# Optimization experiments

Measured on AMD Instinct MI355X. Metric: run time of the kernel, lower is better.

The kernel has to match this reference:

```python
import jax, jax.numpy as jnp
import numpy as np

N_CAND = 10   # n_point_candidate
SIGMA = 1.0   # std threshold for vote filtering
EPS = 1e-6


def _get_pt_candidates(pcld, kpts_ofst, seg, cpt_ofst, k):
    # pcld [b,n,3]; kpts_ofst [b,n,8,3]; seg [b,n,1]; cpt_ofst [b,n,1,3]
    offsets = jnp.concatenate([kpts_ofst, cpt_ofst], axis=2)        # [b,n,9,3]
    scores = jnp.squeeze(seg, axis=-1)                              # [b,n]
    _, idx = jax.lax.top_k(scores, k)                               # [b,k] most confident points
    cands = pcld[:, :, None, :] + offsets                           # [b,n,9,3] candidate kpt positions
    cands = jnp.take_along_axis(cands, idx[:, :, None, None], axis=1)  # [b,k,9,3]
    return jnp.transpose(cands, (0, 2, 1, 3))                       # [b,9,k,3]


def _pts_clustering_with_std(kpts_cans, sigma=SIGMA):
    # kpts_cans [b,n_kpts,k,3]: keep candidates within sigma*std of the mean, average survivors
    mean = jnp.mean(kpts_cans, axis=2, keepdims=True)
    std = jnp.std(kpts_cans, axis=2, keepdims=True)
    inlier = jnp.all(jnp.abs(kpts_cans - mean) <= sigma * std, axis=-1)  # [b,n_kpts,k]
    w = inlier.astype(kpts_cans.dtype)[..., None]
    return jnp.sum(kpts_cans * w, axis=2) / (jnp.sum(w, axis=2) + EPS)   # [b,n_kpts,3]


def _rt_svd_transform(A, B, w):
    # Weighted Kabsch: find R,t with R @ A + t ~= B.  A,B [b,n,3]; w [n]
    wn = w / jnp.sum(w)
    cA = jnp.einsum('n,bnc->bc', wn, A)[:, None, :]                 # weighted centroids
    cB = jnp.einsum('n,bnc->bc', wn, B)[:, None, :]
    Am, Bm = A - cA, B - cB
    H = jnp.einsum('bni,n,bnj->bij', Am, w, Bm)                     # [b,3,3] cross-covariance
    U, S, Vh = jnp.linalg.svd(H)
    V = jnp.swapaxes(Vh, -1, -2)
    R0 = V @ jnp.swapaxes(U, -1, -2)
    flip = jnp.where(jnp.linalg.det(R0) < 0.0, -1.0, 1.0)           # reflection fix
    V = V.at[:, :, -1].multiply(flip[:, None])
    R = V @ jnp.swapaxes(U, -1, -2)                                 # [b,3,3]
    t = jnp.swapaxes(cB, -1, -2) - R @ jnp.swapaxes(cA, -1, -2)     # [b,3,1]
    return R, t


def setup_inputs() -> dict:
    key = jax.random.key(0)
    k1, k2, k3, k4, k5 = jax.random.split(key, 5)
    b, n, nk = 64, 12288, 8
    return {
        'pcld_input': jax.random.normal(k1, (b, n, 3), jnp.float32),
        'kpts_pre_input': jax.random.normal(k2, (b, n, nk, 3), jnp.float32),
        'cpt_pre_input': jax.random.normal(k3, (b, n, 1, 3), jnp.float32),
        'seg_pre_input': jax.random.uniform(k4, (b, n, 1), jnp.float32),
        'mesh_kpts_input': jax.random.normal(k5, (b, nk + 1, 3), jnp.float32),
    }


def reference(pcld_input, kpts_pre_input, cpt_pre_input, seg_pre_input, mesh_kpts_input):
    obj_kpts = _get_pt_candidates(pcld_input, kpts_pre_input, seg_pre_input, cpt_pre_input, N_CAND)
    kpts_voted = _pts_clustering_with_std(obj_kpts)                 # [b,9,3]
    n_pts = kpts_voted.shape[1]
    weights_vector = jnp.ones((n_pts,), dtype=kpts_voted.dtype)
    batch_R, batch_t = _rt_svd_transform(mesh_kpts_input, kpts_voted, weights_vector)
    batch_t = jnp.reshape(batch_t, (-1, 3))
    return batch_R, batch_t, kpts_voted
```

## Files before the change

kernel.cpp:

```cpp
#include <hip/hip_runtime.h>
#include <math.h>

#define NB      64
#define NPTS    12288
#define KTOP    10
#define NKP     9
#define T       1024
#define NWAVES  (T / 64)
#define PERTHD  (NPTS / T)

struct Pair { float v; int i; };

__device__ __forceinline__ bool better(const Pair& a, const Pair& b) {
    return (a.v > b.v) || (a.v == b.v && a.i < b.i);
}

__device__ __forceinline__ void ce(Pair& x, Pair& y) {
    if (better(y, x)) { Pair t = x; x = y; y = t; }
}

template <int LEN>
__device__ __forceinline__ void lane_sort_desc(Pair (&L)[LEN]) {
    #pragma unroll
    for (int r = 0; r < LEN; ++r) {
        #pragma unroll
        for (int i = 0; i + 1 < LEN; i += 2) {
            if ((r & 1) == 0) ce(L[i], L[i + 1]);
        }
        #pragma unroll
        for (int i = 1; i + 1 < LEN; i += 2) {
            if ((r & 1) == 1) ce(L[i], L[i + 1]);
        }
    }
}

template <int LEN>
__device__ __forceinline__ void wave_topk(Pair (&L)[LEN], Pair (&out)[KTOP]) {
    #pragma unroll
    for (int k = 0; k < KTOP; ++k) {
        Pair w = L[0];
        #pragma unroll
        for (int s = 1; s < 64; s <<= 1) {
            Pair o;
            o.v = __shfl_xor(w.v, s);
            o.i = __shfl_xor(w.i, s);
            if (better(o, w)) w = o;
        }
        out[k] = w;
        if (L[0].v == w.v && L[0].i == w.i) {
            #pragma unroll
            for (int i = 0; i + 1 < LEN; ++i) L[i] = L[i + 1];
            L[LEN - 1].v = -INFINITY; L[LEN - 1].i = 0x7fffffff;
        }
    }
}

__global__ __launch_bounds__(T)
void pose_fused(const float* __restrict__ pcld,
                const float* __restrict__ kpts,
                const float* __restrict__ cpt,
                const float* __restrict__ seg,
                const float* __restrict__ mesh,
                float* __restrict__ out)
{
    const int b = blockIdx.x;
    const int t = threadIdx.x;
    const int lane = t & 63;
    const int w = t >> 6;

    __shared__ Pair  wavetop[NWAVES][KTOP];
    __shared__ int   topidx[KTOP];
    __shared__ float cands[NKP][KTOP][3];
    __shared__ float voted[NKP][3];

    const float4* segb4 = (const float4*)(seg + (size_t)b * NPTS);
    Pair L[PERTHD];
    #pragma unroll
    for (int j = 0; j < 3; ++j) {
        int f4 = t + j * T;
        float4 a = segb4[f4];
        L[4 * j + 0] = {a.x, 4 * f4 + 0};
        L[4 * j + 1] = {a.y, 4 * f4 + 1};
        L[4 * j + 2] = {a.z, 4 * f4 + 2};
        L[4 * j + 3] = {a.w, 4 * f4 + 3};
    }
    lane_sort_desc<PERTHD>(L);

    Pair wt[KTOP];
    wave_topk<PERTHD>(L, wt);
    if (lane == 0) {
        #pragma unroll
        for (int j = 0; j < KTOP; ++j) wavetop[w][j] = wt[j];
    }
    __syncthreads();

    if (w == 0) {
        Pair M[KTOP];
        if (lane < NWAVES) {
            #pragma unroll
            for (int j = 0; j < KTOP; ++j) M[j] = wavetop[lane][j];
        } else {
            #pragma unroll
            for (int j = 0; j < KTOP; ++j) { M[j].v = -INFINITY; M[j].i = 0x7fffffff; }
        }
        Pair top[KTOP];
        wave_topk<KTOP>(M, top);
        if (lane == 0) {
            #pragma unroll
            for (int j = 0; j < KTOP; ++j) topidx[j] = top[j].i;
        }
    }
    __syncthreads();

    if (t < NKP * KTOP) {
        int j = t / KTOP;
        int i = t % KTOP;
        int p = topidx[i];
        size_t base = (size_t)b * NPTS + p;
        float px = pcld[base * 3 + 0], py = pcld[base * 3 + 1], pz = pcld[base * 3 + 2];
        float ox, oy, oz;
        if (j < 8) {
            size_t kb = (base * 8 + j) * 3;
            ox = kpts[kb + 0]; oy = kpts[kb + 1]; oz = kpts[kb + 2];
        } else {
            size_t cb = base * 3;
            ox = cpt[cb + 0]; oy = cpt[cb + 1]; oz = cpt[cb + 2];
        }
        cands[j][i][0] = px + ox;
        cands[j][i][1] = py + oy;
        cands[j][i][2] = pz + oz;
    }
    __syncthreads();

    if (t < NKP) {
        float mean[3] = {0.f, 0.f, 0.f};
        for (int i = 0; i < KTOP; ++i)
            for (int c = 0; c < 3; ++c) mean[c] += cands[t][i][c];
        for (int c = 0; c < 3; ++c) mean[c] *= (1.0f / KTOP);
        float var[3] = {0.f, 0.f, 0.f};
        for (int i = 0; i < KTOP; ++i)
            for (int c = 0; c < 3; ++c) { float d = cands[t][i][c] - mean[c]; var[c] += d * d; }
        float sd[3];
        for (int c = 0; c < 3; ++c) sd[c] = sqrtf(var[c] * (1.0f / KTOP));
        float wsum = 0.f, acc[3] = {0.f, 0.f, 0.f};
        for (int i = 0; i < KTOP; ++i) {
            bool in = true;
            for (int c = 0; c < 3; ++c) in = in && (fabsf(cands[t][i][c] - mean[c]) <= sd[c]);
            if (in) {
                wsum += 1.f;
                for (int c = 0; c < 3; ++c) acc[c] += cands[t][i][c];
            }
        }
        float inv = 1.f / (wsum + 1e-6f);
        for (int c = 0; c < 3; ++c) {
            float v = acc[c] * inv;
            voted[t][c] = v;
            out[NB * 9 + NB * 3 + ((size_t)b * NKP + t) * 3 + c] = v;
        }
    }
    __syncthreads();

    if (t == 0) {
        const float* mb = mesh + (size_t)b * NKP * 3;
        float A[NKP][3], Bv[NKP][3];
        float cA[3] = {0, 0, 0}, cB[3] = {0, 0, 0};
        for (int n = 0; n < NKP; ++n) {
            for (int c = 0; c < 3; ++c) {
                A[n][c]  = mb[n * 3 + c];
                Bv[n][c] = voted[n][c];
                cA[c] += A[n][c];
                cB[c] += Bv[n][c];
            }
        }
        for (int c = 0; c < 3; ++c) { cA[c] *= (1.0f / NKP); cB[c] *= (1.0f / NKP); }

        float H[3][3] = {{0,0,0},{0,0,0},{0,0,0}};
        for (int n = 0; n < NKP; ++n)
            for (int i = 0; i < 3; ++i)
                for (int j = 0; j < 3; ++j)
                    H[i][j] += (A[n][i] - cA[i]) * (Bv[n][j] - cB[j]);

        float Km[3][3];
        for (int i = 0; i < 3; ++i)
            for (int j = 0; j < 3; ++j) {
                float s = 0;
                for (int l = 0; l < 3; ++l) s += H[l][i] * H[l][j];
                Km[i][j] = s;
            }

        float V[3][3] = {{1,0,0},{0,1,0},{0,0,1}};
        for (int sweep = 0; sweep < 5; ++sweep) {
            for (int p = 0; p < 2; ++p) {
                for (int q = p + 1; q < 3; ++q) {
                    float apq = Km[p][q];
                    float app = Km[p][p], aqq = Km[q][q];
                    if (fabsf(apq) <= 1e-12f * (fabsf(app) + fabsf(aqq)) || apq == 0.0f) continue;
                    float theta = (aqq - app) / (2.0f * apq);
                    float tj = ((theta >= 0.0f) ? 1.0f : -1.0f) / (fabsf(theta) + sqrtf(theta * theta + 1.0f));
                    float cj = 1.0f / sqrtf(tj * tj + 1.0f);
                    float sj = tj * cj;
                    for (int l = 0; l < 3; ++l) {
                        float klp = Km[l][p], klq = Km[l][q];
                        Km[l][p] = cj * klp - sj * klq;
                        Km[l][q] = sj * klp + cj * klq;
                    }
                    for (int l = 0; l < 3; ++l) {
                        float kpl = Km[p][l], kql = Km[q][l];
                        Km[p][l] = cj * kpl - sj * kql;
                        Km[q][l] = sj * kpl + cj * kql;
                    }
                    for (int l = 0; l < 3; ++l) {
                        float vlp = V[l][p], vlq = V[l][q];
                        V[l][p] = cj * vlp - sj * vlq;
                        V[l][q] = sj * vlp + cj * vlq;
                    }
                }
            }
        }

        float eig[3] = {Km[0][0], Km[1][1], Km[2][2]};
        int ord[3] = {0, 1, 2};
        if (eig[ord[0]] < eig[ord[1]]) { int tmp = ord[0]; ord[0] = ord[1]; ord[1] = tmp; }
        if (eig[ord[1]] < eig[ord[2]]) { int tmp = ord[1]; ord[1] = ord[2]; ord[2] = tmp; }
        if (eig[ord[0]] < eig[ord[1]]) { int tmp = ord[0]; ord[0] = ord[1]; ord[1] = tmp; }

        float detH =
            H[0][0] * (H[1][1] * H[2][2] - H[1][2] * H[2][1]) -
            H[0][1] * (H[1][0] * H[2][2] - H[1][2] * H[2][0]) +
            H[0][2] * (H[1][0] * H[2][1] - H[1][1] * H[2][0]);
        float dsign[3] = {1.0f, 1.0f, (detH < 0.0f) ? -1.0f : 1.0f};

        float R[3][3] = {{0,0,0},{0,0,0},{0,0,0}};
        for (int k = 0; k < 3; ++k) {
            int c = ord[k];
            float s = sqrtf(fmaxf(eig[c], 0.0f));
            float invs = 1.0f / fmaxf(s, 1e-12f);
            float u[3];
            for (int l = 0; l < 3; ++l) {
                float a = 0;
                for (int m = 0; m < 3; ++m) a += H[l][m] * V[m][c];
                u[l] = a * invs;
            }
            for (int r = 0; r < 3; ++r)
                for (int cc = 0; cc < 3; ++cc)
                    R[r][cc] += dsign[k] * V[r][c] * u[cc];
        }

        float tv[3];
        for (int c = 0; c < 3; ++c) {
            float a = 0;
            for (int m = 0; m < 3; ++m) a += R[c][m] * cA[m];
            tv[c] = cB[c] - a;
        }

        for (int r = 0; r < 3; ++r)
            for (int c = 0; c < 3; ++c)
                out[(size_t)b * 9 + r * 3 + c] = R[r][c];
        for (int c = 0; c < 3; ++c)
            out[NB * 9 + (size_t)b * 3 + c] = tv[c];
    }
}

extern "C" void kernel_launch(void* const* d_in, const int* in_sizes, int n_in,
                              void* d_out, int out_size, void* d_ws, size_t ws_size,
                              hipStream_t stream) {
    const float* pcld = (const float*)d_in[0];
    const float* kpts = (const float*)d_in[1];
    const float* cpt  = (const float*)d_in[2];
    const float* seg  = (const float*)d_in[3];
    const float* mesh = (const float*)d_in[4];
    float* out = (float*)d_out;

    pose_fused<<<NB, T, 0, stream>>>(pcld, kpts, cpt, seg, mesh, out);
}
```

Measured before the change: 141.2 us.

## Replace per-lane sort top-k with threshold prefilter and packed 64-bit keys

The top-k selection over segmentation scores now keeps only values at or above a fixed threshold, collecting them into a small shared candidate list with atomics. One wave then picks the top 10 from that list using 64-bit packed value/index keys and max-shuffles. If the candidate count falls outside [KTOP, CAND_MAX], a wave-level exact scan of the whole row runs instead. This drops the per-lane odd-even sort and the two-level Pair reduction. It depends on the score distribution: non-negative floats compare correctly as packed keys, and the slow fallback path costs more when taken.

```diff
diff --git a/kernel.cpp b/kernel.cpp
--- a/kernel.cpp
+++ b/kernel.cpp
@@ -1,59 +1,21 @@
 #include <hip/hip_runtime.h>
 #include <math.h>
+
+typedef unsigned long long u64;
+typedef unsigned int u32;
 
 #define NB      64
 #define NPTS    12288
 #define KTOP    10
 #define NKP     9
 #define T       1024
-#define NWAVES  (T / 64)
-#define PERTHD  (NPTS / T)
-
-struct Pair { float v; int i; };
-
-__device__ __forceinline__ bool better(const Pair& a, const Pair& b) {
-    return (a.v > b.v) || (a.v == b.v && a.i < b.i);
+#define CAND_MAX 128
+#define THETA   0.997f
+
+__device__ __forceinline__ u64 pack(float v, int idx) {
+    return ((u64)__float_as_uint(v) << 32) | (u32)(~idx);
 }
-
-__device__ __forceinline__ void ce(Pair& x, Pair& y) {
-    if (better(y, x)) { Pair t = x; x = y; y = t; }
-}
-
-template <int LEN>
-__device__ __forceinline__ void lane_sort_desc(Pair (&L)[LEN]) {
-    #pragma unroll
-    for (int r = 0; r < LEN; ++r) {
-        #pragma unroll
-        for (int i = 0; i + 1 < LEN; i += 2) {
-            if ((r & 1) == 0) ce(L[i], L[i + 1]);
-        }
-        #pragma unroll
-        for (int i = 1; i + 1 < LEN; i += 2) {
-            if ((r & 1) == 1) ce(L[i], L[i + 1]);
-        }
-    }
-}
-
-template <int LEN>
-__device__ __forceinline__ void wave_topk(Pair (&L)[LEN], Pair (&out)[KTOP]) {
-    #pragma unroll
-    for (int k = 0; k < KTOP; ++k) {
-        Pair w = L[0];
-        #pragma unroll
-        for (int s = 1; s < 64; s <<= 1) {
-            Pair o;
-            o.v = __shfl_xor(w.v, s);
-            o.i = __shfl_xor(w.i, s);
-            if (better(o, w)) w = o;
-        }
-        out[k] = w;
-        if (L[0].v == w.v && L[0].i == w.i) {
-            #pragma unroll
-            for (int i = 0; i + 1 < LEN; ++i) L[i] = L[i + 1];
-            L[LEN - 1].v = -INFINITY; L[LEN - 1].i = 0x7fffffff;
-        }
-    }
-}
+__device__ __forceinline__ int unpack_idx(u64 p) { return (int)(~(u32)p); }
 
 __global__ __launch_bounds__(T)
 void pose_fused(const float* __restrict__ pcld,
@@ -66,48 +28,83 @@
     const int b = blockIdx.x;
     const int t = threadIdx.x;
     const int lane = t & 63;
-    const int w = t >> 6;
-
-    __shared__ Pair  wavetop[NWAVES][KTOP];
+    const int wid = t >> 6;
+
+    __shared__ u64   cand[CAND_MAX];
+    __shared__ int   cnt;
     __shared__ int   topidx[KTOP];
     __shared__ float cands[NKP][KTOP][3];
     __shared__ float voted[NKP][3];
 
+    if (t == 0) cnt = 0;
+    __syncthreads();
+
     const float4* segb4 = (const float4*)(seg + (size_t)b * NPTS);
-    Pair L[PERTHD];
     #pragma unroll
     for (int j = 0; j < 3; ++j) {
         int f4 = t + j * T;
         float4 a = segb4[f4];
-        L[4 * j + 0] = {a.x, 4 * f4 + 0};
-        L[4 * j + 1] = {a.y, 4 * f4 + 1};
-        L[4 * j + 2] = {a.z, 4 * f4 + 2};
-        L[4 * j + 3] = {a.w, 4 * f4 + 3};
-    }
-    lane_sort_desc<PERTHD>(L);
-
-    Pair wt[KTOP];
-    wave_topk<PERTHD>(L, wt);
-    if (lane == 0) {
         #pragma unroll
-        for (int j = 0; j < KTOP; ++j) wavetop[w][j] = wt[j];
-    }
-    __syncthreads();
-
-    if (w == 0) {
-        Pair M[KTOP];
-        if (lane < NWAVES) {
+        for (int c = 0; c < 4; ++c) {
+            float v = (c == 0) ? a.x : (c == 1) ? a.y : (c == 2) ? a.z : a.w;
+            if (v >= THETA) {
+                int slot = atomicAdd(&cnt, 1);
+                if (slot < CAND_MAX) cand[slot] = pack(v, 4 * f4 + c);
+            }
+        }
+    }
+    __syncthreads();
+
+    if (wid == 0) {
+        int n = cnt;
+        if (n >= KTOP && n <= CAND_MAX) {
+            u64 a = (lane     < n) ? cand[lane]      : 0;
+            u64 bq = (lane + 64 < n) ? cand[lane + 64] : 0;
+            u64 hi = a > bq ? a : bq;
+            u64 lo = a > bq ? bq : a;
             #pragma unroll
-            for (int j = 0; j < KTOP; ++j) M[j] = wavetop[lane][j];
+            for (int k = 0; k < KTOP; ++k) {
+                u64 w = hi;
+                #pragma unroll
+                for (int s = 1; s < 64; s <<= 1) {
+                    u64 o = __shfl_xor(w, s);
+                    w = o > w ? o : w;
+                }
+                if (lane == 0) topidx[k] = unpack_idx(w);
+                if (hi == w) { hi = lo; lo = 0; }
+            }
         } else {
+            const float* segb = seg + (size_t)b * NPTS;
+            u64 loc[KTOP];
             #pragma unroll
-            for (int j = 0; j < KTOP; ++j) { M[j].v = -INFINITY; M[j].i = 0x7fffffff; }
-        }
-        Pair top[KTOP];
-        wave_topk<KTOP>(M, top);
-        if (lane == 0) {
+            for (int j = 0; j < KTOP; ++j) loc[j] = 0;
+            for (int i = lane; i < NPTS; i += 64) {
+                u64 p = pack(segb[i], i);
+                if (p > loc[KTOP - 1]) {
+                    loc[KTOP - 1] = p;
+                    #pragma unroll
+                    for (int j = KTOP - 1; j > 0; --j) {
+                        if (loc[j] > loc[j - 1]) { u64 tmp = loc[j]; loc[j] = loc[j - 1]; loc[j - 1] = tmp; }
+                    }
+                }
+            }
+            u64 cur = loc[0];
             #pragma unroll
-            for (int j = 0; j < KTOP; ++j) topidx[j] = top[j].i;
+            for (int k = 0; k < KTOP; ++k) {
+                u64 w = cur;
+                #pragma unroll
+                for (int s = 1; s < 64; s <<= 1) {
+                    u64 o = __shfl_xor(w, s);
+                    w = o > w ? o : w;
+                }
+                if (lane == 0) topidx[k] = unpack_idx(w);
+                if (cur == w) {
+                    #pragma unroll
+                    for (int i = 0; i + 1 < KTOP; ++i) loc[i] = loc[i + 1];
+                    loc[KTOP - 1] = 0;
+                    cur = loc[0];
+                }
+            }
         }
     }
     __syncthreads();
```

Result: faster. 125.4 us (-11.2%).
